# Performance work log

Hardware: AMD Instinct MI355X
Metric: run time of the kernel (lower is better)

The kernel has to match this reference:

```python
import jax, jax.numpy as jnp
import numpy as np

B, S, DIM = 2, 512, 4096
SMAX = 4096
HQ, HKV, HD = 32, 8, 128
REP = HQ // HKV
THETA = 1e6
NEG = -1e9  # stands in for -inf in the causal mask (safe under softmax/vjp)


def setup_inputs() -> dict:
    key = jax.random.key(0)
    ks = jax.random.split(key, 8)
    x = jax.random.normal(ks[0], (B, S, DIM), jnp.float32)
    # RoPE tables (complex freqs_cis represented as cos/sin), rope_theta=1e6
    inv = 1.0 / (THETA ** (np.arange(0, HD, 2, dtype=np.float64) / HD))
    ang = np.arange(SMAX, dtype=np.float64)[:, None] * inv[None, :]
    freqs_cos = jnp.asarray(np.cos(ang), jnp.float32)  # [SMAX, HD//2]
    freqs_sin = jnp.asarray(np.sin(ang), jnp.float32)
    cache = jax.random.normal(ks[1], (2, 1, B, SMAX, HKV, HD), jnp.float32) * 0.02
    i = np.arange(SMAX)
    mask = jnp.asarray(np.where(i[None, :] <= i[:, None], 0.0, NEG), jnp.float32)
    storage_idx = jnp.arange(S, dtype=jnp.int32)
    sc = 0.02
    wq = jax.random.normal(ks[2], (HQ * HD, DIM), jnp.float32) * sc
    wk = jax.random.normal(ks[3], (HKV * HD, DIM), jnp.float32) * sc
    wv = jax.random.normal(ks[4], (HKV * HD, DIM), jnp.float32) * sc
    wo = jax.random.normal(ks[5], (DIM, HQ * HD), jnp.float32) * sc
    return {"x": x, "freqs_cos": freqs_cos, "freqs_sin": freqs_sin, "cache": cache,
            "mask": mask, "storage_idx": storage_idx, "wq": wq, "wk": wk, "wv": wv, "wo": wo}


def _rope(t, c, s):
    # t: [B,S,H,HD]; consecutive pairs (2i, 2i+1) form complex numbers
    tr = t.reshape(*t.shape[:-1], -1, 2)
    a, b = tr[..., 0], tr[..., 1]
    o0 = a * c - b * s
    o1 = a * s + b * c
    return jnp.stack([o0, o1], axis=-1).reshape(t.shape)


def reference(x, freqs_cos, freqs_sin, cache, mask, storage_idx, wq, wk, wv, wo):
    bsz, seqlen, _ = x.shape
    hd = cache.shape[-1]
    hkv = cache.shape[-2]
    hq = wq.shape[0] // hd
    rep = hq // hkv
    xq = (x @ wq.T).reshape(bsz, seqlen, hq, hd)
    xk = (x @ wk.T).reshape(bsz, seqlen, hkv, hd)
    xv = (x @ wv.T).reshape(bsz, seqlen, hkv, hd)
    c = freqs_cos[storage_idx][None, :, None, :]  # [1,S,1,HD//2]
    s = freqs_sin[storage_idx][None, :, None, :]
    xq = _rope(xq, c, s)
    xk = _rope(xk, c, s)
    # rotating-cache write (index_copy along seq dim of cache[0/1, li])
    k_cache = cache[0, 0].at[:, storage_idx].set(xk)  # [B,SMAX,HKV,HD]
    v_cache = cache[1, 0].at[:, storage_idx].set(xv)
    keys = jnp.repeat(k_cache, rep, axis=2)    # GQA expand -> [B,SMAX,HQ,HD]
    values = jnp.repeat(v_cache, rep, axis=2)
    # NOTE: faithful to source: scores = QK^T / (head_dim ** -0.5)
    scores = jnp.einsum('bqhd,bkhd->bhqk', xq, keys) / (hd ** -0.5)
    scores = scores + mask[storage_idx][None, None, :, :]
    probs = jax.nn.softmax(scores.astype(jnp.float32), axis=-1).astype(xq.dtype)
    out = jnp.einsum('bhqk,bkhd->bqhd', probs, values).reshape(bsz, seqlen, hq * hd)
    return out @ wo.T
```

## Files before the change

kernel.cpp:

```cpp
#include <hip/hip_runtime.h>

#define Bn   2
#define Sn   512
#define DIMn 4096
#define HQn  32
#define HKVn 8
#define HDn  128
#define NPAIR 64
#define KVN  (HKVn * HDn)
#define NALL (DIMn + 2 * KVN)
#define SCALE 11.313708498984761f

typedef short bf16x8 __attribute__((ext_vector_type(8)));
typedef float f32x4 __attribute__((ext_vector_type(4)));
typedef unsigned short ushort8 __attribute__((ext_vector_type(8)));
typedef int i32x4 __attribute__((ext_vector_type(4)));

__device__ __forceinline__ unsigned short f2bf_rne(float f) {
  unsigned u = __builtin_bit_cast(unsigned, f);
  u += 0x7fffu + ((u >> 16) & 1u);
  return (unsigned short)(u >> 16);
}
__device__ __forceinline__ float bf2f(unsigned short h) {
  unsigned u = ((unsigned)h) << 16;
  return __builtin_bit_cast(float, u);
}
__device__ __forceinline__ void split_bf16(float x, unsigned short& hi, unsigned short& lo) {
  unsigned u = __builtin_bit_cast(unsigned, x);
  hi = (unsigned short)(u >> 16);
  float hf = __builtin_bit_cast(float, u & 0xffff0000u);
  lo = (unsigned short)(__builtin_bit_cast(unsigned, x - hf) >> 16);
}
__device__ __forceinline__ void gload16(const void* g, void* lds) {
  __builtin_amdgcn_global_load_lds(
      (const __attribute__((address_space(1))) unsigned int*)g,
      (__attribute__((address_space(3))) unsigned int*)lds, 16, 0, 0);
}

__global__ __launch_bounds__(256) void quant_rows(
    const float* __restrict__ x, const float* __restrict__ wq,
    const float* __restrict__ wk, const float* __restrict__ wv,
    signed char* __restrict__ xh8, signed char* __restrict__ xl8,
    signed char* __restrict__ wh8, signed char* __restrict__ wl8,
    float* __restrict__ sA, float* __restrict__ sW)
{
  const int r = blockIdx.x;
  const int t = threadIdx.x;
  const float* src; signed char* ph; signed char* pl; float* ps; size_t prow;
  if (r < 1024) {
    src = x + (size_t)r * DIMn; ph = xh8; pl = xl8; ps = sA + r; prow = (size_t)r * DIMn;
  } else {
    int wr_ = r - 1024;
    ps = sW + wr_; ph = wh8; pl = wl8; prow = (size_t)wr_ * DIMn;
    if (wr_ < DIMn)            src = wq + (size_t)wr_ * DIMn;
    else if (wr_ < DIMn + KVN) src = wk + (size_t)(wr_ - DIMn) * DIMn;
    else                       src = wv + (size_t)(wr_ - DIMn - KVN) * DIMn;
  }
  float4 v[4];
  float am = 0.f;
  #pragma unroll
  for (int j = 0; j < 4; ++j) {
    v[j] = ((const float4*)src)[t + j * 256];
    am = fmaxf(am, fmaxf(fmaxf(fabsf(v[j].x), fabsf(v[j].y)),
                         fmaxf(fabsf(v[j].z), fabsf(v[j].w))));
  }
  #pragma unroll
  for (int o = 1; o < 64; o <<= 1) am = fmaxf(am, __shfl_xor(am, o));
  __shared__ float wm[4];
  if ((t & 63) == 0) wm[t >> 6] = am;
  __syncthreads();
  am = fmaxf(fmaxf(wm[0], wm[1]), fmaxf(wm[2], wm[3]));
  const float inv = (am > 0.f) ? 32512.0f / am : 0.f;
  if (t == 0) *ps = am * (1.0f / 32512.0f);
  #pragma unroll
  for (int j = 0; j < 4; ++j) {
    float fv[4] = {v[j].x, v[j].y, v[j].z, v[j].w};
    signed char hh[4], ll[4];
    #pragma unroll
    for (int e = 0; e < 4; ++e) {
      int q = __float2int_rn(fv[e] * inv);
      int hi = (q + 128) >> 8;
      hh[e] = (signed char)hi;
      ll[e] = (signed char)(q - (hi << 8));
    }
    ((char4*)(ph + prow))[t + j * 256] = make_char4(hh[0], hh[1], hh[2], hh[3]);
    ((char4*)(pl + prow))[t + j * 256] = make_char4(ll[0], ll[1], ll[2], ll[3]);
  }
}

__global__ void conv_plain_k(const float* __restrict__ s, unsigned short* __restrict__ hi, int n8)
{
  for (int i = blockIdx.x * blockDim.x + threadIdx.x; i < n8; i += gridDim.x * blockDim.x) {
    float4 a = ((const float4*)s)[2 * i];
    float4 b = ((const float4*)s)[2 * i + 1];
    float xv[8] = {a.x, a.y, a.z, a.w, b.x, b.y, b.z, b.w};
    ushort8 h;
    #pragma unroll
    for (int j = 0; j < 8; ++j) h[j] = f2bf_rne(xv[j]);
    ((ushort8*)hi)[i] = h;
  }
}

__global__ __launch_bounds__(256, 3) void qkv_gemm_i8(
    const signed char* __restrict__ Ah, const signed char* __restrict__ Al,
    const signed char* __restrict__ Wh, const signed char* __restrict__ Wl,
    const float* __restrict__ sA, const float* __restrict__ sW,
    float* __restrict__ CQ, float* __restrict__ CK, unsigned short* __restrict__ CV)
{
  constexpr int KS = 64;
  constexpr int TILEB = 192 * 128;
  __shared__ __align__(16) signed char Ls[2][TILEB];

  const int t = threadIdx.x, w = t >> 6, lane = t & 63;
  const int bid = blockIdx.x;
  const int s = (bid & 7) * 96 + (bid >> 3);
  const int by = s & 7, bx = s >> 3;
  const int bm = by * 128, bn = bx * 64;

  const signed char* gsrc[6];
  int ldst[6];
  #pragma unroll
  for (int j = 0; j < 6; ++j) {
    int u = j * 256 + t;
    int R = u >> 3, slot = u & 7;
    int q = slot ^ (R & 7);
    const signed char* base = (R < 128) ? (q < 4 ? Ah : Al) : (q < 4 ? Wh : Wl);
    int rg = (R < 128) ? (bm + R) : (bn + (R - 128));
    gsrc[j] = base + (size_t)rg * DIMn + (q & 3) * 16;
    ldst[j] = u * 16;
  }

  const int wr = w >> 1, wc = w & 1;
  const int rl = lane & 15, kh = lane >> 4;
  int aoff[4], boff[2];
  #pragma unroll
  for (int fm = 0; fm < 4; ++fm) {
    int R = wr * 64 + fm * 16 + rl;
    aoff[fm] = R * 128 + ((kh ^ (R & 7)) * 16);
  }
  #pragma unroll
  for (int fn = 0; fn < 2; ++fn) {
    int R = 128 + wc * 32 + fn * 16 + rl;
    boff[fn] = R * 128 + ((kh ^ (R & 7)) * 16);
  }

  i32x4 acc1[4][2], acc2[4][2];
  #pragma unroll
  for (int i = 0; i < 4; ++i)
  #pragma unroll
    for (int j = 0; j < 2; ++j) {
      acc1[i][j] = (i32x4){0, 0, 0, 0};
      acc2[i][j] = (i32x4){0, 0, 0, 0};
    }

  #pragma unroll
  for (int j = 0; j < 6; ++j) gload16(gsrc[j], &Ls[0][ldst[j]]);

  for (int tt = 0; tt < DIMn / KS; ++tt) {
    asm volatile("s_waitcnt vmcnt(0)" ::: "memory");
    __builtin_amdgcn_s_barrier();
    __builtin_amdgcn_sched_barrier(0);
    const int buf = tt & 1;
    if (tt + 1 < DIMn / KS) {
      #pragma unroll
      for (int j = 0; j < 6; ++j)
        gload16(gsrc[j] + (size_t)(tt + 1) * KS, &Ls[buf ^ 1][ldst[j]]);
    }
    const signed char* Lp = &Ls[buf][0];
    i32x4 ah[4], al[4], bh[2], bl[2];
    #pragma unroll
    for (int fm = 0; fm < 4; ++fm) {
      ah[fm] = *(const i32x4*)(Lp + aoff[fm]);
      al[fm] = *(const i32x4*)(Lp + (aoff[fm] ^ 64));
    }
    #pragma unroll
    for (int fn = 0; fn < 2; ++fn) {
      bh[fn] = *(const i32x4*)(Lp + boff[fn]);
      bl[fn] = *(const i32x4*)(Lp + (boff[fn] ^ 64));
    }
    __builtin_amdgcn_s_setprio(1);
    #pragma unroll
    for (int fm = 0; fm < 4; ++fm)
    #pragma unroll
      for (int fn = 0; fn < 2; ++fn) {
        acc1[fm][fn] = __builtin_amdgcn_mfma_i32_16x16x64_i8(ah[fm], bh[fn], acc1[fm][fn], 0, 0, 0);
        acc2[fm][fn] = __builtin_amdgcn_mfma_i32_16x16x64_i8(ah[fm], bl[fn], acc2[fm][fn], 0, 0, 0);
        acc2[fm][fn] = __builtin_amdgcn_mfma_i32_16x16x64_i8(al[fm], bh[fn], acc2[fm][fn], 0, 0, 0);
      }
    __builtin_amdgcn_s_setprio(0);
  }

  #pragma unroll
  for (int fn = 0; fn < 2; ++fn) {
    const int colW = bn + wc * 32 + fn * 16 + rl;
    const float sw = sW[colW];
    #pragma unroll
    for (int fm = 0; fm < 4; ++fm) {
      #pragma unroll
      for (int j = 0; j < 4; ++j) {
        int grow = bm + wr * 64 + fm * 16 + kh * 4 + j;
        float val = sA[grow] * sw *
            fmaf((float)acc1[fm][fn][j], 65536.0f, (float)acc2[fm][fn][j] * 256.0f);
        if (colW < DIMn)            CQ[(size_t)grow * DIMn + colW] = val;
        else if (colW < DIMn + KVN) CK[(size_t)grow * KVN + (colW - DIMn)] = val;
        else                        CV[(size_t)grow * KVN + (colW - DIMn - KVN)] = f2bf_rne(val);
      }
    }
  }
}

template<bool SPLIT, int OMODE>
__global__ __launch_bounds__(256, 2) void pgemm3(
    const unsigned short* __restrict__ Ah, const unsigned short* __restrict__ Al,
    const unsigned short* __restrict__ Wh, const unsigned short* __restrict__ Wl,
    void* __restrict__ C0, void* __restrict__ C1, void* __restrict__ C2, int Kd)
{
  constexpr int BM = 128, BN = 64;
  constexpr int ROWS = BM + BN;
  constexpr int UPT = ROWS / 32;
  constexpr int KS = SPLIT ? 32 : 64;
  constexpr int TILEB = ROWS * 128;

  __shared__ __align__(16) unsigned char Ls[3 * TILEB];

  const int t = threadIdx.x, w = t >> 6, lane = t & 63;
  const int bid = blockIdx.x;
  const int s = (bid & 7) * 64 + (bid >> 3);
  const int bm = (s & 7) * BM, bn = (s >> 3) * BN;

  const unsigned short* gsrc[UPT];
  #pragma unroll
  for (int j = 0; j < UPT; ++j) {
    int u = j * 256 + t;
    int R = u >> 3;
    int q = (u & 7) ^ (R & 7);
    int chunk = SPLIT ? (q & 3) : q;
    bool lo_ = SPLIT && (q >= 4);
    const unsigned short* base = (R < BM) ? (lo_ ? Al : Ah) : (lo_ ? Wl : Wh);
    int rg = (R < BM) ? (bm + R) : (bn + (R - BM));
    gsrc[j] = base + (size_t)rg * Kd + chunk * 8;
  }

  const int wr = w >> 1, wc = w & 1;
  const int rl = lane & 15, kh = lane >> 4;
  int aoff[4], boff[2];
  #pragma unroll
  for (int fm = 0; fm < 4; ++fm) {
    int r = wr * 64 + fm * 16 + rl;
    aoff[fm] = r * 128 + ((kh ^ (r & 7)) * 16);
  }
  #pragma unroll
  for (int fn = 0; fn < 2; ++fn) {
    int r = BM + wc * 32 + fn * 16 + rl;
    boff[fn] = r * 128 + ((kh ^ (r & 7)) * 16);
  }

  f32x4 acc[4][2];
  #pragma unroll
  for (int i = 0; i < 4; ++i)
  #pragma unroll
    for (int j = 0; j < 2; ++j) acc[i][j] = (f32x4){0.f, 0.f, 0.f, 0.f};

  const int nt = Kd / KS;
  #pragma unroll
  for (int j = 0; j < UPT; ++j) gload16(gsrc[j], &Ls[0 * TILEB + (j * 256 + t) * 16]);
  #pragma unroll
  for (int j = 0; j < UPT; ++j) gload16(gsrc[j] + KS, &Ls[1 * TILEB + (j * 256 + t) * 16]);

  int cur = 0;
  for (int tt = 0; tt < nt; ++tt) {
    if (tt + 1 < nt) asm volatile("s_waitcnt vmcnt(%0)" :: "n"(UPT) : "memory");
    else             asm volatile("s_waitcnt vmcnt(0)" ::: "memory");
    __builtin_amdgcn_s_barrier();
    __builtin_amdgcn_sched_barrier(0);

    int pre = cur + 2; if (pre >= 3) pre -= 3;
    if (tt + 2 < nt) {
      #pragma unroll
      for (int j = 0; j < UPT; ++j)
        gload16(gsrc[j] + (size_t)(tt + 2) * KS, &Ls[pre * TILEB + (j * 256 + t) * 16]);
    }

    const unsigned char* Lp = &Ls[cur * TILEB];
    bf16x8 a0[4], a1[4], b0[2], b1[2];
    #pragma unroll
    for (int fm = 0; fm < 4; ++fm) {
      a0[fm] = *(const bf16x8*)(Lp + aoff[fm]);
      a1[fm] = *(const bf16x8*)(Lp + (aoff[fm] ^ 64));
    }
    #pragma unroll
    for (int fn = 0; fn < 2; ++fn) {
      b0[fn] = *(const bf16x8*)(Lp + boff[fn]);
      b1[fn] = *(const bf16x8*)(Lp + (boff[fn] ^ 64));
    }
    __builtin_amdgcn_s_setprio(1);
    #pragma unroll
    for (int fm = 0; fm < 4; ++fm)
    #pragma unroll
      for (int fn = 0; fn < 2; ++fn) {
        if constexpr (SPLIT) {
          acc[fm][fn] = __builtin_amdgcn_mfma_f32_16x16x32_bf16(a0[fm], b0[fn], acc[fm][fn], 0, 0, 0);
          acc[fm][fn] = __builtin_amdgcn_mfma_f32_16x16x32_bf16(a1[fm], b0[fn], acc[fm][fn], 0, 0, 0);
          acc[fm][fn] = __builtin_amdgcn_mfma_f32_16x16x32_bf16(a0[fm], b1[fn], acc[fm][fn], 0, 0, 0);
        } else {
          acc[fm][fn] = __builtin_amdgcn_mfma_f32_16x16x32_bf16(a0[fm], b0[fn], acc[fm][fn], 0, 0, 0);
          acc[fm][fn] = __builtin_amdgcn_mfma_f32_16x16x32_bf16(a1[fm], b1[fn], acc[fm][fn], 0, 0, 0);
        }
      }
    __builtin_amdgcn_s_setprio(0);
    cur += 1; if (cur >= 3) cur -= 3;
  }

  const int crow0 = bm + wr * 64 + kh * 4;
  #pragma unroll
  for (int fm = 0; fm < 4; ++fm)
  #pragma unroll
    for (int fn = 0; fn < 2; ++fn)
    #pragma unroll
      for (int j = 0; j < 4; ++j) {
        int row = crow0 + fm * 16 + j;
        float v = acc[fm][fn][j];
        int col = bn + wc * 32 + fn * 16 + rl;
        if constexpr (OMODE == 0) {
          ((float*)C0)[(size_t)row * DIMn + col] = v;
        } else {
          if (col < DIMn)
            ((float*)C0)[(size_t)row * DIMn + col] = v;
          else if (col < DIMn + KVN)
            ((float*)C1)[(size_t)row * KVN + (col - DIMn)] = v;
          else
            ((unsigned short*)C2)[(size_t)row * KVN + (col - DIMn - KVN)] = f2bf_rne(v);
        }
      }
}

template<bool SPLIT, int BN>
__global__ __launch_bounds__(256, 2) void gemm_mfma(
    const float* __restrict__ A,
    const float* __restrict__ W0, float* __restrict__ C0,
    const float* __restrict__ W1, float* __restrict__ C1,
    int Kd, int N)
{
  constexpr int BM = 64;
  constexpr int KSTEP = SPLIT ? 32 : 64;
  constexpr int CPR = SPLIT ? 4 : 8;
  constexpr int AUNITS = BM * KSTEP / 8;
  constexpr int UNITS  = (BM + BN) * KSTEP / 8;
  constexpr int UPT = UNITS / 256;
  constexpr int FN = BN / 32;
  constexpr int ROWS = BM + BN;

  __shared__ __align__(16) unsigned short Ls[2][ROWS * 64];

  const float* __restrict__ W = (blockIdx.z == 0) ? W0 : W1;
  float* __restrict__ Cp = (blockIdx.z == 0) ? C0 : C1;

  const int t  = threadIdx.x;
  const int bm = blockIdx.y * BM;
  const int bn = blockIdx.x * BN;

  const float* gsrc[UPT];
  int loff[UPT];
  #pragma unroll
  for (int i = 0; i < UPT; ++i) {
    int u = i * 256 + t;
    int row, c;
    if (u < AUNITS) {
      row = u / CPR; c = u % CPR;
      gsrc[i] = A + (size_t)(bm + row) * Kd + c * 8;
    } else {
      int v = u - AUNITS;
      int rr = v / CPR; c = v % CPR;
      row = BM + rr;
      gsrc[i] = W + (size_t)(bn + rr) * Kd + c * 8;
    }
    loff[i] = row * 64 + (c ^ (row & 7)) * 8;
  }

  const int lane = t & 63;
  const int w  = t >> 6;
  const int wr = w >> 1, wc = w & 1;
  const int rl = lane & 15, kh = lane >> 4;

  int aoff[2], boff[FN];
  #pragma unroll
  for (int fm = 0; fm < 2; ++fm) {
    int row = wr * 32 + fm * 16 + rl;
    aoff[fm] = row * 64 + (kh ^ (row & 7)) * 8;
  }
  #pragma unroll
  for (int fn = 0; fn < FN; ++fn) {
    int row = BM + wc * (BN / 2) + fn * 16 + rl;
    boff[fn] = row * 64 + (kh ^ (row & 7)) * 8;
  }

  f32x4 acc[2][FN];
  #pragma unroll
  for (int i = 0; i < 2; ++i)
  #pragma unroll
    for (int j = 0; j < FN; ++j) acc[i][j] = (f32x4){0.f, 0.f, 0.f, 0.f};

  float4 f0[UPT], f1[UPT];
  #pragma unroll
  for (int i = 0; i < UPT; ++i) {
    f0[i] = *(const float4*)(gsrc[i]);
    f1[i] = *(const float4*)(gsrc[i] + 4);
  }

  const int nt = Kd / KSTEP;
  for (int tt = 0; tt < nt; ++tt) {
    unsigned short* Lp = &Ls[tt & 1][0];
    #pragma unroll
    for (int i = 0; i < UPT; ++i) {
      float xv[8] = {f0[i].x, f0[i].y, f0[i].z, f0[i].w,
                     f1[i].x, f1[i].y, f1[i].z, f1[i].w};
      ushort8 hi, lo;
      #pragma unroll
      for (int j = 0; j < 8; ++j) {
        if constexpr (SPLIT) {
          unsigned short h_, l_;
          split_bf16(xv[j], h_, l_);
          hi[j] = h_; lo[j] = l_;
        } else {
          hi[j] = f2bf_rne(xv[j]);
          lo[j] = 0;
        }
      }
      *(ushort8*)(Lp + loff[i]) = hi;
      if constexpr (SPLIT)
        *(ushort8*)(((uintptr_t)(Lp + loff[i])) ^ 64) = lo;
    }
    if (tt + 1 < nt) {
      #pragma unroll
      for (int i = 0; i < UPT; ++i) {
        f0[i] = *(const float4*)(gsrc[i] + (size_t)(tt + 1) * KSTEP);
        f1[i] = *(const float4*)(gsrc[i] + (size_t)(tt + 1) * KSTEP + 4);
      }
    }
    __syncthreads();

    bf16x8 a0[2], a1[2], b0[FN], b1[FN];
    #pragma unroll
    for (int fm = 0; fm < 2; ++fm) {
      const unsigned short* p = Lp + aoff[fm];
      a0[fm] = *(const bf16x8*)p;
      a1[fm] = *(const bf16x8*)(((uintptr_t)p) ^ 64);
    }
    #pragma unroll
    for (int fn = 0; fn < FN; ++fn) {
      const unsigned short* p = Lp + boff[fn];
      b0[fn] = *(const bf16x8*)p;
      b1[fn] = *(const bf16x8*)(((uintptr_t)p) ^ 64);
    }
    #pragma unroll
    for (int fm = 0; fm < 2; ++fm)
    #pragma unroll
      for (int fn = 0; fn < FN; ++fn) {
        if constexpr (SPLIT) {
          acc[fm][fn] = __builtin_amdgcn_mfma_f32_16x16x32_bf16(a0[fm], b0[fn], acc[fm][fn], 0, 0, 0);
          acc[fm][fn] = __builtin_amdgcn_mfma_f32_16x16x32_bf16(a1[fm], b0[fn], acc[fm][fn], 0, 0, 0);
          acc[fm][fn] = __builtin_amdgcn_mfma_f32_16x16x32_bf16(a0[fm], b1[fn], acc[fm][fn], 0, 0, 0);
        } else {
          acc[fm][fn] = __builtin_amdgcn_mfma_f32_16x16x32_bf16(a0[fm], b0[fn], acc[fm][fn], 0, 0, 0);
          acc[fm][fn] = __builtin_amdgcn_mfma_f32_16x16x32_bf16(a1[fm], b1[fn], acc[fm][fn], 0, 0, 0);
        }
      }
  }

  const int crow0 = bm + wr * 32 + kh * 4;
  const int ccol0 = bn + wc * (BN / 2) + rl;
  #pragma unroll
  for (int fm = 0; fm < 2; ++fm)
  #pragma unroll
    for (int fn = 0; fn < FN; ++fn)
    #pragma unroll
      for (int j = 0; j < 4; ++j)
        Cp[(size_t)(crow0 + fm * 16 + j) * N + ccol0 + fn * 16] = acc[fm][fn][j];
}

#define KT 32

template<bool BF16IO>
__global__ __launch_bounds__(256, 2) void flash_attn_mfma(
    const float* __restrict__ Qg, const float* __restrict__ Kg, const void* __restrict__ Vgv,
    const float* __restrict__ fc, const float* __restrict__ fs,
    const int* __restrict__ sidx, void* __restrict__ Ov)
{
  const int bid = blockIdx.x;
  const int qt = bid & 7;
  const int h  = (bid >> 3) & 31;
  const int b  = bid >> 8;
  const int q0 = qt * 64;
  const int hk = h >> 2;

  __shared__ __align__(16) unsigned short Ks[2][2][32][128];
  __shared__ __align__(16) unsigned short Vt[2][128][40];

  const int t = threadIdx.x;
  const int w = t >> 6;
  const int lane = t & 63;
  const int rl = lane & 15;
  const int kh = lane >> 4;

  const int qrow = q0 + w * 16 + rl;
  const int qp = sidx[qrow];

  int kr[2], kc_[2];
  #pragma unroll
  for (int i = 0; i < 2; ++i) { int u = i * 256 + t; kr[i] = u >> 4; kc_[i] = u & 15; }
  const int kkv = t >> 3, dcv = t & 7;

  const int nkt = (q0 + 64) / KT;
  const int qmaxw = q0 + w * 16 + 15;

  float kreg[2][8]; float4 kc4[2], ks4[2];
  float vregf[16];
  ushort8 vregu[2];

  #pragma unroll
  for (int i = 0; i < 2; ++i) {
    const float* kp_ = Kg + ((size_t)(b * Sn + kr[i]) * HKVn + hk) * HDn + kc_[i] * 8;
    *(float4*)&kreg[i][0] = *(const float4*)kp_;
    *(float4*)&kreg[i][4] = *(const float4*)(kp_ + 4);
    int posk = sidx[kr[i]];
    kc4[i] = *(const float4*)(fc + (size_t)posk * NPAIR + kc_[i] * 4);
    ks4[i] = *(const float4*)(fs + (size_t)posk * NPAIR + kc_[i] * 4);
  }
  if constexpr (BF16IO) {
    const unsigned short* vp_ = (const unsigned short*)Vgv +
        ((size_t)(b * Sn + kkv) * HKVn + hk) * HDn + dcv * 16;
    vregu[0] = *(const ushort8*)vp_;
    vregu[1] = *(const ushort8*)(vp_ + 8);
  } else {
    const float* vp_ = (const float*)Vgv + ((size_t)(b * Sn + kkv) * HKVn + hk) * HDn + dcv * 16;
    #pragma unroll
    for (int i = 0; i < 4; ++i) *(float4*)&vregf[i * 4] = *(const float4*)(vp_ + i * 4);
  }

  bf16x8 qh[4], ql[4];
  {
    const float* qptr = Qg + ((size_t)(b * Sn + qrow) * HQn + h) * HDn;
    #pragma unroll
    for (int ds = 0; ds < 4; ++ds) {
      int d0 = ds * 32 + kh * 8;
      float4 u0 = *(const float4*)(qptr + d0);
      float4 u1 = *(const float4*)(qptr + d0 + 4);
      float4 c4 = *(const float4*)(fc + (size_t)qp * NPAIR + d0 / 2);
      float4 s4 = *(const float4*)(fs + (size_t)qp * NPAIR + d0 / 2);
      float v[8];
      v[0] = u0.x * c4.x - u0.y * s4.x;  v[1] = u0.x * s4.x + u0.y * c4.x;
      v[2] = u0.z * c4.y - u0.w * s4.y;  v[3] = u0.z * s4.y + u0.w * c4.y;
      v[4] = u1.x * c4.z - u1.y * s4.z;  v[5] = u1.x * s4.z + u1.y * c4.z;
      v[6] = u1.z * c4.w - u1.w * s4.w;  v[7] = u1.z * s4.w + u1.w * c4.w;
      #pragma unroll
      for (int j = 0; j < 8; ++j) {
        unsigned short h_, l_;
        split_bf16(v[j], h_, l_);
        qh[ds][j] = (short)h_; ql[ds][j] = (short)l_;
      }
    }
  }

  float m_run = -3.0e38f, l_run = 0.f;
  f32x4 acc_o[8];
  #pragma unroll
  for (int i = 0; i < 8; ++i) acc_o[i] = (f32x4){0.f, 0.f, 0.f, 0.f};

  for (int tt = 0; tt < nkt; ++tt) {
    const int kbase = tt * KT;
    const int buf = tt & 1;

    #pragma unroll
    for (int i = 0; i < 2; ++i) {
      float rv[8];
      rv[0] = kreg[i][0] * kc4[i].x - kreg[i][1] * ks4[i].x;
      rv[1] = kreg[i][0] * ks4[i].x + kreg[i][1] * kc4[i].x;
      rv[2] = kreg[i][2] * kc4[i].y - kreg[i][3] * ks4[i].y;
      rv[3] = kreg[i][2] * ks4[i].y + kreg[i][3] * kc4[i].y;
      rv[4] = kreg[i][4] * kc4[i].z - kreg[i][5] * ks4[i].z;
      rv[5] = kreg[i][4] * ks4[i].z + kreg[i][5] * kc4[i].z;
      rv[6] = kreg[i][6] * kc4[i].w - kreg[i][7] * ks4[i].w;
      rv[7] = kreg[i][6] * ks4[i].w + kreg[i][7] * kc4[i].w;
      ushort8 hi, lo;
      #pragma unroll
      for (int j = 0; j < 8; ++j) {
        unsigned short h_, l_;
        split_bf16(rv[j], h_, l_);
        hi[j] = h_; lo[j] = l_;
      }
      int slot = kc_[i] ^ (kr[i] & 15);
      *(ushort8*)&Ks[buf][0][kr[i]][slot * 8] = hi;
      *(ushort8*)&Ks[buf][1][kr[i]][slot * 8] = lo;
    }
    if constexpr (BF16IO) {
      #pragma unroll
      for (int i = 0; i < 8; ++i) {
        Vt[buf][dcv * 16 + i][kkv] = vregu[0][i];
        Vt[buf][dcv * 16 + 8 + i][kkv] = vregu[1][i];
      }
    } else {
      #pragma unroll
      for (int i = 0; i < 16; ++i)
        Vt[buf][dcv * 16 + i][kkv] = f2bf_rne(vregf[i]);
    }

    if (tt + 1 < nkt) {
      const int kb = kbase + KT;
      #pragma unroll
      for (int i = 0; i < 2; ++i) {
        const float* kp_ = Kg + ((size_t)(b * Sn + kb + kr[i]) * HKVn + hk) * HDn + kc_[i] * 8;
        *(float4*)&kreg[i][0] = *(const float4*)kp_;
        *(float4*)&kreg[i][4] = *(const float4*)(kp_ + 4);
        int posk = sidx[kb + kr[i]];
        kc4[i] = *(const float4*)(fc + (size_t)posk * NPAIR + kc_[i] * 4);
        ks4[i] = *(const float4*)(fs + (size_t)posk * NPAIR + kc_[i] * 4);
      }
      if constexpr (BF16IO) {
        const unsigned short* vp_ = (const unsigned short*)Vgv +
            ((size_t)(b * Sn + kb + kkv) * HKVn + hk) * HDn + dcv * 16;
        vregu[0] = *(const ushort8*)vp_;
        vregu[1] = *(const ushort8*)(vp_ + 8);
      } else {
        const float* vp_ = (const float*)Vgv + ((size_t)(b * Sn + kb + kkv) * HKVn + hk) * HDn + dcv * 16;
        #pragma unroll
        for (int i = 0; i < 4; ++i) *(float4*)&vregf[i * 4] = *(const float4*)(vp_ + i * 4);
      }
    }
    __syncthreads();

    if (kbase > qmaxw) continue;

    float p[8];
    #pragma unroll
    for (int fm = 0; fm < 2; ++fm) {
      f32x4 accs = (f32x4){0.f, 0.f, 0.f, 0.f};
      #pragma unroll
      for (int ds = 0; ds < 4; ++ds) {
        int slot = (ds * 4 + kh) ^ rl;
        bf16x8 kH = *(const bf16x8*)&Ks[buf][0][fm * 16 + rl][slot * 8];
        bf16x8 kL = *(const bf16x8*)&Ks[buf][1][fm * 16 + rl][slot * 8];
        accs = __builtin_amdgcn_mfma_f32_16x16x32_bf16(kH, qh[ds], accs, 0, 0, 0);
        accs = __builtin_amdgcn_mfma_f32_16x16x32_bf16(kL, qh[ds], accs, 0, 0, 0);
        accs = __builtin_amdgcn_mfma_f32_16x16x32_bf16(kH, ql[ds], accs, 0, 0, 0);
      }
      #pragma unroll
      for (int r = 0; r < 4; ++r) {
        int kp = kbase + fm * 16 + kh * 4 + r;
        p[fm * 4 + r] = accs[r] * SCALE + ((kp <= qp) ? 0.f : -1.0e9f);
      }
    }

    float tmax = p[0];
    #pragma unroll
    for (int i = 1; i < 8; ++i) tmax = fmaxf(tmax, p[i]);
    tmax = fmaxf(tmax, __shfl_xor(tmax, 16));
    tmax = fmaxf(tmax, __shfl_xor(tmax, 32));
    float m_new = fmaxf(m_run, tmax);
    float crs = __expf(m_run - m_new);
    m_run = m_new;
    float tsum = 0.f;
    bf16x8 pa;
    #pragma unroll
    for (int i = 0; i < 8; ++i) {
      float ev = __expf(p[i] - m_new);
      tsum += ev;
      pa[i] = (short)f2bf_rne(ev);
    }
    tsum += __shfl_xor(tsum, 16);
    tsum += __shfl_xor(tsum, 32);
    l_run = l_run * crs + tsum;

    float cq[4];
    #pragma unroll
    for (int r = 0; r < 4; ++r) cq[r] = __shfl(crs, kh * 4 + r);

    #pragma unroll
    for (int db = 0; db < 8; ++db) {
      short4 v0 = *(const short4*)&Vt[buf][db * 16 + rl][kh * 4];
      short4 v1 = *(const short4*)&Vt[buf][db * 16 + rl][16 + kh * 4];
      bf16x8 vb = {v0.x, v0.y, v0.z, v0.w, v1.x, v1.y, v1.z, v1.w};
      f32x4 a = acc_o[db];
      a[0] *= cq[0]; a[1] *= cq[1]; a[2] *= cq[2]; a[3] *= cq[3];
      acc_o[db] = __builtin_amdgcn_mfma_f32_16x16x32_bf16(pa, vb, a, 0, 0, 0);
    }
  }

  float lq[4];
  #pragma unroll
  for (int r = 0; r < 4; ++r) lq[r] = 1.0f / __shfl(l_run, kh * 4 + r);
  #pragma unroll
  for (int db = 0; db < 8; ++db)
  #pragma unroll
    for (int r = 0; r < 4; ++r) {
      int q = q0 + w * 16 + kh * 4 + r;
      size_t idx = ((size_t)(b * Sn + q) * HQn + h) * HDn + db * 16 + rl;
      float val = acc_o[db][r] * lq[r];
      if constexpr (BF16IO) ((unsigned short*)Ov)[idx] = f2bf_rne(val);
      else                  ((float*)Ov)[idx] = val;
    }
}

extern "C" void kernel_launch(void* const* d_in, const int* in_sizes, int n_in,
                              void* d_out, int out_size, void* d_ws, size_t ws_size,
                              hipStream_t stream)
{
  const float* x    = (const float*)d_in[0];
  const float* fc   = (const float*)d_in[1];
  const float* fs   = (const float*)d_in[2];
  const int*   sidx = (const int*)d_in[5];
  const float* wq   = (const float*)d_in[6];
  const float* wk   = (const float*)d_in[7];
  const float* wv   = (const float*)d_in[8];
  const float* wo   = (const float*)d_in[9];
  float* out = (float*)d_out;

  const int M = Bn * Sn;
  const size_t EX  = (size_t)M * DIMn;
  const size_t EW  = (size_t)DIMn * DIMn;
  const size_t EK  = (size_t)M * KVN;
  const size_t EX8 = EX;
  const size_t EW8 = (size_t)NALL * DIMn;

  char* p = (char*)d_ws;
  signed char* xh8 = (signed char*)p;        p += EX8;
  signed char* xl8 = (signed char*)p;        p += EX8;
  signed char* wh8 = (signed char*)p;        p += EW8;
  signed char* wl8 = (signed char*)p;        p += EW8;
  float* sA = (float*)p;                     p += 1024 * 4;
  float* sW = (float*)p;                     p += (size_t)NALL * 4;
  float* Qw = (float*)p;                     p += 4 * EX;
  float* Kw = (float*)p;                     p += 4 * EK;
  unsigned short* Vw = (unsigned short*)p;   p += 2 * EK;
  unsigned short* woh = (unsigned short*)p;  p += 2 * EW;
  unsigned short* Aw = (unsigned short*)p;   p += 2 * EX;
  const size_t NEED = (size_t)(p - (char*)d_ws);

  if (ws_size >= NEED) {
    quant_rows<<<1024 + NALL, 256, 0, stream>>>(
        x, wq, wk, wv, xh8, xl8, wh8, wl8, sA, sW);
    qkv_gemm_i8<<<768, 256, 0, stream>>>(
        xh8, xl8, wh8, wl8, sA, sW, Qw, Kw, Vw);
    conv_plain_k<<<1024, 256, 0, stream>>>(wo, woh, (int)(EW / 8));
    flash_attn_mfma<true><<<Bn * HQn * (Sn / 64), 256, 0, stream>>>(
        Qw, Kw, Vw, fc, fs, sidx, Aw);
    pgemm3<false, 0><<<512, 256, 0, stream>>>(
        Aw, Aw, woh, woh, out, nullptr, nullptr, DIMn);
  } else {
    float* Qw2 = (float*)d_ws;
    float* Kw2 = Qw2 + (size_t)M * HQn * HDn;
    float* Vw2 = Kw2 + (size_t)M * HKVn * HDn;
    float* Aw2 = Vw2 + (size_t)M * HKVn * HDn;
    gemm_mfma<true, 128><<<dim3(DIMn / 128, M / 64, 1), 256, 0, stream>>>(
        x, wq, Qw2, wq, Qw2, DIMn, DIMn);
    gemm_mfma<true, 64><<<dim3((HKVn * HDn) / 64, M / 64, 2), 256, 0, stream>>>(
        x, wk, Kw2, wv, Vw2, DIMn, HKVn * HDn);
    flash_attn_mfma<false><<<Bn * HQn * (Sn / 64), 256, 0, stream>>>(
        Qw2, Kw2, Vw2, fc, fs, sidx, Aw2);
    gemm_mfma<false, 128><<<dim3(DIMn / 128, M / 64, 1), 256, 0, stream>>>(
        Aw2, wo, out, wo, out, DIMn, DIMn);
  }
}
```

Before: 235.4 us.

## Widen QKV int8 GEMM N-tile to 96 with split-phase B loading

Grows the QKV int8 GEMM block tile from 128x64 to 128x96 and cuts the grid from 768 to 512 blocks, so each block reuses its A tile across more output columns and total global/LDS traffic for A goes down. Each K step is split into two phases with their own waitcnt and barrier: the first 6 loads plus MFMAs on two B fragments, then a seventh load overlapped with MFMAs on the third fragment. This uses more LDS and registers (launch bounds drop from 3 to 2 waves per SIMD) and adds a barrier per iteration, which may lower occupancy and latency hiding.

```diff
diff --git a/kernel.cpp b/kernel.cpp
--- a/kernel.cpp
+++ b/kernel.cpp
@@ -101,98 +101,132 @@
   }
 }
 
-__global__ __launch_bounds__(256, 3) void qkv_gemm_i8(
+__global__ __launch_bounds__(256, 2) void qkv_gemm_i8(
     const signed char* __restrict__ Ah, const signed char* __restrict__ Al,
     const signed char* __restrict__ Wh, const signed char* __restrict__ Wl,
     const float* __restrict__ sA, const float* __restrict__ sW,
     float* __restrict__ CQ, float* __restrict__ CK, unsigned short* __restrict__ CV)
 {
   constexpr int KS = 64;
-  constexpr int TILEB = 192 * 128;
+  constexpr int TILEB = 224 * 128;
   __shared__ __align__(16) signed char Ls[2][TILEB];
 
   const int t = threadIdx.x, w = t >> 6, lane = t & 63;
   const int bid = blockIdx.x;
-  const int s = (bid & 7) * 96 + (bid >> 3);
-  const int by = s & 7, bx = s >> 3;
-  const int bm = by * 128, bn = bx * 64;
-
-  const signed char* gsrc[6];
-  int ldst[6];
-  #pragma unroll
-  for (int j = 0; j < 6; ++j) {
+  const int s = (bid & 7) * 64 + (bid >> 3);
+  const int bx = s >> 3, by = s & 7;
+  const int bm = by * 128, bn = bx * 96;
+
+  const signed char* gsrc[7];
+  int ldst[7];
+  #pragma unroll
+  for (int j = 0; j < 4; ++j) {
     int u = j * 256 + t;
     int R = u >> 3, slot = u & 7;
     int q = slot ^ (R & 7);
-    const signed char* base = (R < 128) ? (q < 4 ? Ah : Al) : (q < 4 ? Wh : Wl);
-    int rg = (R < 128) ? (bm + R) : (bn + (R - 128));
-    gsrc[j] = base + (size_t)rg * DIMn + (q & 3) * 16;
+    gsrc[j] = (q < 4 ? Ah : Al) + (size_t)(bm + R) * DIMn + (q & 3) * 16;
     ldst[j] = u * 16;
+  }
+  #pragma unroll
+  for (int j = 4; j < 7; ++j) {
+    int rb;
+    if (j == 4)      rb = (t >> 3);
+    else if (j == 5) rb = 48 + (t >> 3);
+    else             rb = ((t < 128) ? 32 : 64) + (t >> 3);
+    int slot = t & 7;
+    int q = slot ^ (rb & 7);
+    gsrc[j] = (q < 4 ? Wh : Wl) + (size_t)(bn + rb) * DIMn + (q & 3) * 16;
+    ldst[j] = (128 + rb) * 128 + slot * 16;
   }
 
   const int wr = w >> 1, wc = w & 1;
   const int rl = lane & 15, kh = lane >> 4;
-  int aoff[4], boff[2];
+  int aoff[4], boff[3];
   #pragma unroll
   for (int fm = 0; fm < 4; ++fm) {
     int R = wr * 64 + fm * 16 + rl;
     aoff[fm] = R * 128 + ((kh ^ (R & 7)) * 16);
   }
   #pragma unroll
-  for (int fn = 0; fn < 2; ++fn) {
-    int R = 128 + wc * 32 + fn * 16 + rl;
+  for (int fn = 0; fn < 3; ++fn) {
+    int R = 128 + wc * 48 + fn * 16 + rl;
     boff[fn] = R * 128 + ((kh ^ (R & 7)) * 16);
   }
 
-  i32x4 acc1[4][2], acc2[4][2];
+  i32x4 acc1[4][3], acc2[4][3];
   #pragma unroll
   for (int i = 0; i < 4; ++i)
   #pragma unroll
-    for (int j = 0; j < 2; ++j) {
+    for (int j = 0; j < 3; ++j) {
       acc1[i][j] = (i32x4){0, 0, 0, 0};
       acc2[i][j] = (i32x4){0, 0, 0, 0};
     }
 
-  #pragma unroll
-  for (int j = 0; j < 6; ++j) gload16(gsrc[j], &Ls[0][ldst[j]]);
-
-  for (int tt = 0; tt < DIMn / KS; ++tt) {
-    asm volatile("s_waitcnt vmcnt(0)" ::: "memory");
+  const int nt = DIMn / KS;
+  #pragma unroll
+  for (int j = 0; j < 7; ++j) gload16(gsrc[j], &Ls[0][ldst[j]]);
+
+  for (int tt = 0; tt < nt; ++tt) {
+    const int buf = tt & 1, nbuf = buf ^ 1;
+    const bool more = (tt + 1 < nt);
+
+    asm volatile("s_waitcnt vmcnt(1)" ::: "memory");
     __builtin_amdgcn_s_barrier();
     __builtin_amdgcn_sched_barrier(0);
-    const int buf = tt & 1;
-    if (tt + 1 < DIMn / KS) {
+    if (more) {
       #pragma unroll
       for (int j = 0; j < 6; ++j)
-        gload16(gsrc[j] + (size_t)(tt + 1) * KS, &Ls[buf ^ 1][ldst[j]]);
+        gload16(gsrc[j] + (size_t)(tt + 1) * KS, &Ls[nbuf][ldst[j]]);
     }
     const signed char* Lp = &Ls[buf][0];
-    i32x4 ah[4], al[4], bh[2], bl[2];
+    i32x4 ah[4], al[4];
     #pragma unroll
     for (int fm = 0; fm < 4; ++fm) {
       ah[fm] = *(const i32x4*)(Lp + aoff[fm]);
       al[fm] = *(const i32x4*)(Lp + (aoff[fm] ^ 64));
     }
-    #pragma unroll
-    for (int fn = 0; fn < 2; ++fn) {
-      bh[fn] = *(const i32x4*)(Lp + boff[fn]);
-      bl[fn] = *(const i32x4*)(Lp + (boff[fn] ^ 64));
-    }
-    __builtin_amdgcn_s_setprio(1);
-    #pragma unroll
-    for (int fm = 0; fm < 4; ++fm)
-    #pragma unroll
+    {
+      i32x4 bh[2], bl[2];
+      #pragma unroll
       for (int fn = 0; fn < 2; ++fn) {
-        acc1[fm][fn] = __builtin_amdgcn_mfma_i32_16x16x64_i8(ah[fm], bh[fn], acc1[fm][fn], 0, 0, 0);
-        acc2[fm][fn] = __builtin_amdgcn_mfma_i32_16x16x64_i8(ah[fm], bl[fn], acc2[fm][fn], 0, 0, 0);
-        acc2[fm][fn] = __builtin_amdgcn_mfma_i32_16x16x64_i8(al[fm], bh[fn], acc2[fm][fn], 0, 0, 0);
-      }
-    __builtin_amdgcn_s_setprio(0);
-  }
-
-  #pragma unroll
-  for (int fn = 0; fn < 2; ++fn) {
-    const int colW = bn + wc * 32 + fn * 16 + rl;
+        bh[fn] = *(const i32x4*)(Lp + boff[fn]);
+        bl[fn] = *(const i32x4*)(Lp + (boff[fn] ^ 64));
+      }
+      __builtin_amdgcn_s_setprio(1);
+      #pragma unroll
+      for (int fm = 0; fm < 4; ++fm)
+      #pragma unroll
+        for (int fn = 0; fn < 2; ++fn) {
+          acc1[fm][fn] = __builtin_amdgcn_mfma_i32_16x16x64_i8(ah[fm], bh[fn], acc1[fm][fn], 0, 0, 0);
+          acc2[fm][fn] = __builtin_amdgcn_mfma_i32_16x16x64_i8(ah[fm], bl[fn], acc2[fm][fn], 0, 0, 0);
+          acc2[fm][fn] = __builtin_amdgcn_mfma_i32_16x16x64_i8(al[fm], bh[fn], acc2[fm][fn], 0, 0, 0);
+        }
+      __builtin_amdgcn_s_setprio(0);
+    }
+
+    if (more) asm volatile("s_waitcnt vmcnt(6)" ::: "memory");
+    else      asm volatile("s_waitcnt vmcnt(0)" ::: "memory");
+    __builtin_amdgcn_s_barrier();
+    __builtin_amdgcn_sched_barrier(0);
+    if (more)
+      gload16(gsrc[6] + (size_t)(tt + 1) * KS, &Ls[nbuf][ldst[6]]);
+    {
+      i32x4 bh = *(const i32x4*)(Lp + boff[2]);
+      i32x4 bl = *(const i32x4*)(Lp + (boff[2] ^ 64));
+      __builtin_amdgcn_s_setprio(1);
+      #pragma unroll
+      for (int fm = 0; fm < 4; ++fm) {
+        acc1[fm][2] = __builtin_amdgcn_mfma_i32_16x16x64_i8(ah[fm], bh, acc1[fm][2], 0, 0, 0);
+        acc2[fm][2] = __builtin_amdgcn_mfma_i32_16x16x64_i8(ah[fm], bl, acc2[fm][2], 0, 0, 0);
+        acc2[fm][2] = __builtin_amdgcn_mfma_i32_16x16x64_i8(al[fm], bh, acc2[fm][2], 0, 0, 0);
+      }
+      __builtin_amdgcn_s_setprio(0);
+    }
+  }
+
+  #pragma unroll
+  for (int fn = 0; fn < 3; ++fn) {
+    const int colW = bn + wc * 48 + fn * 16 + rl;
     const float sw = sW[colW];
     #pragma unroll
     for (int fm = 0; fm < 4; ++fm) {
@@ -738,7 +772,7 @@
   if (ws_size >= NEED) {
     quant_rows<<<1024 + NALL, 256, 0, stream>>>(
         x, wq, wk, wv, xh8, xl8, wh8, wl8, sA, sW);
-    qkv_gemm_i8<<<768, 256, 0, stream>>>(
+    qkv_gemm_i8<<<512, 256, 0, stream>>>(
         xh8, xl8, wh8, wl8, sA, sW, Qw, Kw, Vw);
     conv_plain_k<<<1024, 256, 0, stream>>>(wo, woh, (int)(EW / 8));
     flash_attn_mfma<true><<<Bn * HQn * (Sn / 64), 256, 0, stream>>>(
```

Result: faster. 219.2 us (-6.9%).
